# Kernel optimization log

Hardware: AMD Instinct MI355X
Metric: run time of the kernel (lower is better)

Reference implementation:

```python
import jax, jax.numpy as jnp
import numpy as np

D = 64        # GatedGraphConv out_channels
N_LAYERS = 5  # number of stacked convs


def setup_inputs() -> dict:
    key = jax.random.key(0)
    ks = jax.random.split(key, 16)
    N, E, G = 100000, 1600000, 64
    s = 0.1
    inp = {
        'conv_weight': jax.random.normal(ks[0], (N_LAYERS, D, D), jnp.float32) * s,
        'gru_w_ih':    jax.random.normal(ks[1], (N_LAYERS, 3 * D, D), jnp.float32) * s,
        'gru_w_hh':    jax.random.normal(ks[2], (N_LAYERS, 3 * D, D), jnp.float32) * s,
        'gru_b_ih':    jax.random.normal(ks[3], (N_LAYERS, 3 * D), jnp.float32) * s,
        'gru_b_hh':    jax.random.normal(ks[4], (N_LAYERS, 3 * D), jnp.float32) * s,
        'fc1_w': jax.random.normal(ks[5], (32, D), jnp.float32) * s,
        'fc1_b': jax.random.normal(ks[6], (32,), jnp.float32) * s,
        'fc2_w': jax.random.normal(ks[7], (16, 32), jnp.float32) * s,
        'fc2_b': jax.random.normal(ks[8], (16,), jnp.float32) * s,
        'fc3_w': jax.random.normal(ks[9], (1, 16), jnp.float32) * s,
        'fc3_b': jax.random.normal(ks[10], (1,), jnp.float32) * s,
        'edge_index': jax.random.randint(ks[11], (2, E), 0, N, jnp.int64 if jax.config.jax_enable_x64 else jnp.int32),
        'batch': jnp.sort(jax.random.randint(ks[12], (N,), 0, G, jnp.int32)),
        'num_nodes': N,
        'num_graphs': G,
    }
    return inp


def _gru_cell(m, h, w_ih, w_hh, b_ih, b_hh):
    # torch.nn.GRUCell math; m: [N,D] input, h: [N,D] hidden
    gi = m @ w_ih.T + b_ih   # [N, 3D]
    gh = h @ w_hh.T + b_hh   # [N, 3D]
    i_r, i_z, i_n = jnp.split(gi, 3, axis=1)
    h_r, h_z, h_n = jnp.split(gh, 3, axis=1)
    r = jax.nn.sigmoid(i_r + h_r)
    z = jax.nn.sigmoid(i_z + h_z)
    n = jnp.tanh(i_n + r * h_n)
    return (1.0 - z) * n + z * h


def reference(conv_weight, gru_w_ih, gru_w_hh, gru_b_ih, gru_b_hh,
              fc1_w, fc1_b, fc2_w, fc2_b, fc3_w, fc3_b,
              edge_index, batch, num_nodes, num_graphs):
    src, dst = edge_index[0], edge_index[1]  # source_to_target flow
    # initial node features: zeros [N,8] zero-padded to D by GatedGraphConv
    x0 = jnp.zeros((num_nodes, D), jnp.float32)

    def step(x, params):
        w, wih, whh, bih, bhh = params
        m = x @ w                                        # [N, D]
        agg = jax.ops.segment_sum(m[src], dst, num_segments=num_nodes)  # scatter-add
        return _gru_cell(agg, x, wih, whh, bih, bhh), None

    x, _ = jax.lax.scan(step, x0,
                        (conv_weight, gru_w_ih, gru_w_hh, gru_b_ih, gru_b_hh))

    # scatter_add pooling over batch -> [num_graphs, D]
    g = jax.ops.segment_sum(x, batch, num_segments=num_graphs)
    h = jax.nn.elu(g @ fc1_w.T + fc1_b)
    h = jax.nn.elu(h @ fc2_w.T + fc2_b)
    return h @ fc3_w.T + fc3_b  # [num_graphs, 1]
```

## Files before the change

### kernel.cpp

```cpp
#include <hip/hip_runtime.h>
#include <math.h>

typedef _Float16 f16x2 __attribute__((ext_vector_type(2)));
typedef _Float16 f16x4 __attribute__((ext_vector_type(4)));
typedef _Float16 f16x8 __attribute__((ext_vector_type(8)));
typedef float f32x4 __attribute__((ext_vector_type(4)));

#define CBITS 10
#define FCHUNK 4096
#define MATSZ 13056
__device__ __forceinline__ int woff(int row) { return 64 * row + 8 * (row >> 1); }

__device__ __forceinline__ float sigmoidf_(float v) {
  return 1.0f / (1.0f + __expf(-v));
}
__device__ __forceinline__ float tanhf_(float v) {
  v = fminf(fmaxf(v, -15.f), 15.f);
  float e = __expf(2.f * v);
  return (e - 1.f) / (e + 1.f);
}
__device__ __forceinline__ float eluf_(float v) { return v > 0.f ? v : (__expf(v) - 1.f); }

__global__ __launch_bounds__(256) void fuse_w_kernel(const float* __restrict__ conv_w,
                                                     const float* __restrict__ w_ih,
                                                     _Float16* __restrict__ wcS) {
  const int l = blockIdx.x >> 2;
  const int j0 = (blockIdx.x & 3) * 48;
  const float* W = conv_w + (size_t)l * 4096;
  const float* wi = w_ih + (size_t)l * 12288;
  _Float16* out = wcS + (size_t)l * MATSZ;
  __shared__ float sWt[64 * 68];
  __shared__ float sI[48 * 64];
  const int t = threadIdx.x;
  for (int i = t; i < 4096; i += 256) sWt[(i & 63) * 68 + (i >> 6)] = W[i];
  for (int i = t; i < 3072; i += 256) sI[i] = wi[j0 * 64 + i];
  __syncthreads();
#pragma unroll
  for (int r = 0; r < 3; ++r) {
    int u = t + 256 * r;
    int j = u >> 4, cg = (u & 15) * 4;
    float4 a = {0.f, 0.f, 0.f, 0.f};
    for (int k = 0; k < 64; ++k) {
      float4 w = *(const float4*)(sWt + k * 68 + cg);
      float s = sI[j * 64 + k];
      a.x += w.x * s; a.y += w.y * s; a.z += w.z * s; a.w += w.w * s;
    }
    int row = j0 + j;
    f16x4 hv;
    hv[0] = (_Float16)a.x; hv[1] = (_Float16)a.y;
    hv[2] = (_Float16)a.z; hv[3] = (_Float16)a.w;
    *(f16x4*)(out + woff(row) + cg) = hv;
  }
}

__global__ __launch_bounds__(256) void whh_prep_kernel(const float* __restrict__ whh,
                                                       _Float16* __restrict__ whhS) {
  int idx = blockIdx.x * 256 + threadIdx.x;
  if (idx >= 15360) return;
  int l = idx / 3072, rem = idx % 3072;
  int r = rem >> 4, c4 = (rem & 15) * 4;
  float4 v = *(const float4*)(whh + (size_t)l * 12288 + r * 64 + c4);
  f16x4 hv;
  hv[0] = (_Float16)v.x; hv[1] = (_Float16)v.y;
  hv[2] = (_Float16)v.z; hv[3] = (_Float16)v.w;
  *(f16x4*)(whhS + (size_t)l * MATSZ + woff(r) + c4) = hv;
}

__global__ __launch_bounds__(256) void bucket_hist_kernel(const int* __restrict__ dst,
                                                          int* __restrict__ bh, int E) {
  __shared__ int h[128];
  const int t = threadIdx.x;
  if (t < 128) h[t] = 0;
  __syncthreads();
  for (int e = blockIdx.x * 256 + t; e < E; e += gridDim.x * 256)
    atomicAdd(&h[dst[e] >> CBITS], 1);
  __syncthreads();
  if (t < 128 && h[t]) atomicAdd(&bh[t * 16], h[t]);
}

__global__ __launch_bounds__(128) void bucket_scan_kernel(int* __restrict__ bh, int nbk,
                                                          int* __restrict__ boffs, int E) {
  __shared__ int s[128];
  const int t = threadIdx.x;
  int v = (t < nbk) ? bh[t * 16] : 0;
  s[t] = v;
  __syncthreads();
  for (int o = 1; o < 128; o <<= 1) {
    int a = (t >= o) ? s[t - o] : 0;
    __syncthreads();
    s[t] += a;
    __syncthreads();
  }
  if (t < nbk) {
    int ex = s[t] - v;
    boffs[t] = ex;
    bh[t * 16] = ex;
  }
  if (t == 0) boffs[nbk] = E;
}

__global__ __launch_bounds__(256) void bucket_fill_kernel(const int* __restrict__ src,
                                                          const int* __restrict__ dst,
                                                          int* __restrict__ bcur,
                                                          unsigned* __restrict__ pairs, int E) {
  __shared__ uint2 staged[FCHUNK];
  __shared__ int h[128], lbase[128], gbase[128], lcur[128];
  const int t = threadIdx.x;
  const int e0 = blockIdx.x * FCHUNK;
  int cnt = E - e0;
  if (cnt > FCHUNK) cnt = FCHUNK;
  if (t < 128) h[t] = 0;
  __syncthreads();
  for (int i = t; i < cnt; i += 256) atomicAdd(&h[dst[e0 + i] >> CBITS], 1);
  __syncthreads();
  if (t < 128) lcur[t] = h[t];
  __syncthreads();
  for (int o = 1; o < 128; o <<= 1) {
    int a = 0;
    if (t < 128 && t >= o) a = lcur[t - o];
    __syncthreads();
    if (t < 128) lcur[t] += a;
    __syncthreads();
  }
  if (t < 128) {
    int ex = lcur[t] - h[t];
    lbase[t] = ex;
    if (h[t]) gbase[t] = atomicAdd(&bcur[t * 16], h[t]);
    lcur[t] = ex;
  }
  __syncthreads();
  for (int i = t; i < cnt; i += 256) {
    int d = dst[e0 + i];
    int b = d >> CBITS;
    int p = atomicAdd(&lcur[b], 1);
    staged[p] = make_uint2((unsigned)src[e0 + i], (unsigned)d);
  }
  __syncthreads();
  for (int i = t; i < cnt; i += 256) {
    uint2 pr = staged[i];
    int b = (int)(pr.y >> CBITS);
    pairs[gbase[b] + (i - lbase[b])] = (pr.x << CBITS) | (pr.y & ((1u << CBITS) - 1));
  }
}

__global__ __launch_bounds__(256) void csr_build_kernel(const unsigned* __restrict__ pairs,
                                                        const int* __restrict__ boffs,
                                                        int* __restrict__ offs,
                                                        int* __restrict__ srcs, int N, int E) {
  const int b = blockIdx.x, t = threadIdx.x;
  const int nbase = b << CBITS;
  __shared__ int deg[1024];
  __shared__ int ssc[256];
  for (int i = t; i < 1024; i += 256) deg[i] = 0;
  __syncthreads();
  const int beg = boffs[b], end = boffs[b + 1];
  for (int e = beg + t; e < end; e += 256) atomicAdd(&deg[pairs[e] & 1023], 1);
  __syncthreads();
  int d0 = deg[4 * t], d1 = deg[4 * t + 1], d2 = deg[4 * t + 2], d3 = deg[4 * t + 3];
  int s = d0 + d1 + d2 + d3;
  ssc[t] = s;
  __syncthreads();
  for (int o = 1; o < 256; o <<= 1) {
    int a = (t >= o) ? ssc[t - o] : 0;
    __syncthreads();
    ssc[t] += a;
    __syncthreads();
  }
  int base = beg + ssc[t] - s;
  int c0 = base, c1 = c0 + d0, c2 = c1 + d1, c3 = c2 + d2;
  if (nbase + 4 * t + 0 < N) offs[nbase + 4 * t + 0] = c0;
  if (nbase + 4 * t + 1 < N) offs[nbase + 4 * t + 1] = c1;
  if (nbase + 4 * t + 2 < N) offs[nbase + 4 * t + 2] = c2;
  if (nbase + 4 * t + 3 < N) offs[nbase + 4 * t + 3] = c3;
  deg[4 * t] = c0; deg[4 * t + 1] = c1; deg[4 * t + 2] = c2; deg[4 * t + 3] = c3;
  if (b == 0 && t == 0) offs[N] = E;
  if (b == 0 && t < 64) srcs[E + t] = 0;
  __syncthreads();
  for (int e = beg + t; e < end; e += 256) {
    unsigned p = pairs[e];
    int pos = atomicAdd(&deg[p & 1023], 1);
    srcs[pos] = (int)(p >> CBITS);
  }
}

__global__ __launch_bounds__(64) void h1_kernel(const float* __restrict__ b_ih,
                                                const float* __restrict__ b_hh,
                                                float* __restrict__ h1) {
  int d = threadIdx.x;
  float r = sigmoidf_(b_ih[d] + b_hh[d]);
  float z = sigmoidf_(b_ih[64 + d] + b_hh[64 + d]);
  float n = tanhf_(b_ih[128 + d] + r * b_hh[128 + d]);
  h1[d] = (1.f - z) * n;
}

__global__ __launch_bounds__(256) void bcast_kernel(const int* __restrict__ offs,
                                                    const float* __restrict__ h1,
                                                    _Float16* __restrict__ xh,
                                                    _Float16* __restrict__ aggh,
                                                    int N, int units) {
  int idx = blockIdx.x * 256 + threadIdx.x;
  if (idx >= units) return;
  int v = idx >> 5, lp = idx & 31;
  float2 hh = *(const float2*)(h1 + lp * 2);
  f16x2 hv;
  hv[0] = (_Float16)hh.x; hv[1] = (_Float16)hh.y;
  *(f16x2*)(xh + (size_t)idx * 2) = hv;
  float dg = (v < N) ? (float)(offs[v + 1] - offs[v]) : 0.f;
  f16x2 av;
  av[0] = (_Float16)(dg * hh.x); av[1] = (_Float16)(dg * hh.y);
  *(f16x2*)(aggh + (size_t)idx * 2) = av;
}

__global__ __launch_bounds__(256) void agg_kernel(const _Float16* __restrict__ xh,
                                                  const int* __restrict__ offs,
                                                  const int* __restrict__ srcs,
                                                  _Float16* __restrict__ aggh, int N) {
  int wave = threadIdx.x >> 6, lane = threadIdx.x & 63;
  int v = blockIdx.x * 4 + wave;
  if (v >= N) return;
  const int beg = offs[v], end = offs[v + 1];
  const int deg = end - beg;
  const int og = lane >> 3;
  const int lp = lane & 7;
  f16x8 acc = {};
  for (int base = 0; base < deg; base += 64) {
    const int cnt = min(64, deg - base);
    int sidx = srcs[beg + base + lane];
    for (int e = 0; e < cnt; e += 8) {
      int me = e + og;
      int s = __shfl(sidx, me);
      f16x8 vv = *(const f16x8*)(xh + (size_t)s * 64 + lp * 8);
      if (me < cnt) acc += vv;
    }
  }
#pragma unroll
  for (int off = 8; off < 64; off <<= 1) {
    union { f16x8 h; int i[4]; } a, b;
    a.h = acc;
#pragma unroll
    for (int w = 0; w < 4; ++w) b.i[w] = __shfl_xor(a.i[w], off);
    acc += b.h;
  }
  if (og == 0) *(f16x8*)(aggh + (size_t)v * 64 + lp * 8) = acc;
}

__global__ __launch_bounds__(256) void gru_kernel(const _Float16* __restrict__ aggh,
                                                  const _Float16* __restrict__ xh_in,
                                                  _Float16* __restrict__ xh_out,
                                                  const _Float16* __restrict__ wcS,
                                                  const _Float16* __restrict__ whhS,
                                                  const float* __restrict__ b_ih,
                                                  const float* __restrict__ b_hh,
                                                  int N, int numIter) {
  __shared__ _Float16 sW[2 * MATSZ];
  const int t = threadIdx.x;
  for (int i = t; i < 2 * (MATSZ / 8); i += 256) {
    int mat = (i >= MATSZ / 8);
    int idx = i - mat * (MATSZ / 8);
    *(f16x8*)(sW + mat * MATSZ + idx * 8) =
        *(const f16x8*)((mat ? whhS : wcS) + idx * 8);
  }
  __syncthreads();
  const int wave = t >> 6, lane = t & 63;
  const int q = lane >> 4, c = lane & 15;
  float bRZ[4], bZZ[4], bIN[4], bHN[4];
#pragma unroll
  for (int dt = 0; dt < 4; ++dt) {
    int d = dt * 16 + c;
    bRZ[dt] = b_ih[d] + b_hh[d];
    bZZ[dt] = b_ih[64 + d] + b_hh[64 + d];
    bIN[dt] = b_ih[128 + d];
    bHN[dt] = b_hh[128 + d];
  }
  f16x8 idf[2];
#pragma unroll
  for (int p = 0; p < 2; ++p) {
    int tgt = p * 16 + c - q * 8;
#pragma unroll
    for (int j = 0; j < 8; ++j) idf[p][j] = (j == tgt) ? (_Float16)1.0f : (_Float16)0.0f;
  }
#pragma unroll 1
  for (int it = blockIdx.x; it < numIter; it += gridDim.x) {
    const int tile = it >> 1, half = it & 1;
    const int nb0 = tile * 64 + wave * 16;
    const size_t rowbase = (size_t)(nb0 + c) * 64;
    f16x8 aA[2], aH[2];
#pragma unroll
    for (int ks = 0; ks < 2; ++ks) {
      aA[ks] = *(const f16x8*)(aggh + rowbase + ks * 32 + q * 8);
      aH[ks] = *(const f16x8*)(xh_in + rowbase + ks * 32 + q * 8);
    }
    f32x4 aR[2], aZ[2], aN[2], aHNa[2], aHO[2];
#pragma unroll
    for (int p = 0; p < 2; ++p) {
      float brz = half ? bRZ[2 + p] : bRZ[p];
      float bzz = half ? bZZ[2 + p] : bZZ[p];
      float bin = half ? bIN[2 + p] : bIN[p];
      float bhn = half ? bHN[2 + p] : bHN[p];
      aR[p] = (f32x4){brz, brz, brz, brz};
      aZ[p] = (f32x4){bzz, bzz, bzz, bzz};
      aN[p] = (f32x4){bin, bin, bin, bin};
      aHNa[p] = (f32x4){bhn, bhn, bhn, bhn};
      aHO[p] = (f32x4){0.f, 0.f, 0.f, 0.f};
    }
#pragma unroll
    for (int ks = 0; ks < 2; ++ks) {
      const int colo = ks * 32 + q * 8;
#pragma unroll
      for (int p = 0; p < 2; ++p) {
        const int r0 = (half * 2 + p) * 16 + c;
        f16x8 bWr = *(const f16x8*)(sW + woff(r0) + colo);
        f16x8 bHr = *(const f16x8*)(sW + MATSZ + woff(r0) + colo);
        f16x8 bWz = *(const f16x8*)(sW + woff(64 + r0) + colo);
        f16x8 bHz = *(const f16x8*)(sW + MATSZ + woff(64 + r0) + colo);
        f16x8 bWn = *(const f16x8*)(sW + woff(128 + r0) + colo);
        f16x8 bHn = *(const f16x8*)(sW + MATSZ + woff(128 + r0) + colo);
        aR[p] = __builtin_amdgcn_mfma_f32_16x16x32_f16(aA[ks], bWr, aR[p], 0, 0, 0);
        aR[p] = __builtin_amdgcn_mfma_f32_16x16x32_f16(aH[ks], bHr, aR[p], 0, 0, 0);
        aZ[p] = __builtin_amdgcn_mfma_f32_16x16x32_f16(aA[ks], bWz, aZ[p], 0, 0, 0);
        aZ[p] = __builtin_amdgcn_mfma_f32_16x16x32_f16(aH[ks], bHz, aZ[p], 0, 0, 0);
        aN[p] = __builtin_amdgcn_mfma_f32_16x16x32_f16(aA[ks], bWn, aN[p], 0, 0, 0);
        aHNa[p] = __builtin_amdgcn_mfma_f32_16x16x32_f16(aH[ks], bHn, aHNa[p], 0, 0, 0);
      }
    }
#pragma unroll
    for (int p = 0; p < 2; ++p)
      aHO[p] = __builtin_amdgcn_mfma_f32_16x16x32_f16(aH[half], idf[p], aHO[p], 0, 0, 0);
#pragma unroll
    for (int p = 0; p < 2; ++p) {
      int d = (half * 2 + p) * 16 + c;
#pragma unroll
      for (int r = 0; r < 4; ++r) {
        int node = nb0 + q * 4 + r;
        if (node < N) {
          float rr = sigmoidf_(aR[p][r]);
          float zz = sigmoidf_(aZ[p][r]);
          float nn = tanhf_(aN[p][r] + rr * aHNa[p][r]);
          float out = nn + zz * (aHO[p][r] - nn);
          xh_out[(size_t)node * 64 + d] = (_Float16)out;
        }
      }
    }
  }
}

__global__ __launch_bounds__(256) void pool_kernel(const _Float16* __restrict__ xh,
                                                   const int* __restrict__ batch,
                                                   float* __restrict__ g, int N) {
  int wave = threadIdx.x >> 6, lane = threadIdx.x & 63;
  int n0 = blockIdx.x * 64 + wave * 16;
  if (n0 >= N) return;
  int end = n0 + 16;
  if (end > N) end = N;
  int cur = batch[n0];
  float acc = 0.f;
  for (int n = n0; n < end; ++n) {
    int b = batch[n];
    if (b != cur) {
      atomicAdd(&g[(size_t)cur * 64 + lane], acc);
      acc = 0.f;
      cur = b;
    }
    acc += (float)xh[(size_t)n * 64 + lane];
  }
  atomicAdd(&g[(size_t)cur * 64 + lane], acc);
}

__global__ __launch_bounds__(256) void mlp_kernel(const float* __restrict__ g,
                                                  const float* __restrict__ w1,
                                                  const float* __restrict__ b1,
                                                  const float* __restrict__ w2,
                                                  const float* __restrict__ b2,
                                                  const float* __restrict__ w3,
                                                  const float* __restrict__ b3,
                                                  float* __restrict__ out, int G) {
  __shared__ float sG[64 * 64];
  __shared__ float sH1[64 * 32];
  __shared__ float sH2[64 * 16];
  int t = threadIdx.x;
  for (int i = t; i < G * 64; i += 256) sG[i] = g[i];
  __syncthreads();
  for (int o = t; o < G * 32; o += 256) {
    int gi = o >> 5, i = o & 31;
    float a = b1[i];
    for (int k = 0; k < 64; ++k) a += sG[gi * 64 + k] * w1[i * 64 + k];
    sH1[gi * 32 + i] = eluf_(a);
  }
  __syncthreads();
  for (int o = t; o < G * 16; o += 256) {
    int gi = o >> 4, i = o & 15;
    float a = b2[i];
    for (int k = 0; k < 32; ++k) a += sH1[gi * 32 + k] * w2[i * 32 + k];
    sH2[gi * 16 + i] = eluf_(a);
  }
  __syncthreads();
  for (int o = t; o < G; o += 256) {
    float a = b3[0];
    for (int k = 0; k < 16; ++k) a += sH2[o * 16 + k] * w3[k];
    out[o] = a;
  }
}

extern "C" void kernel_launch(void* const* d_in, const int* in_sizes, int n_in,
                              void* d_out, int out_size, void* d_ws, size_t ws_size,
                              hipStream_t stream) {
  const float* conv_w = (const float*)d_in[0];
  const float* w_ih = (const float*)d_in[1];
  const float* w_hh = (const float*)d_in[2];
  const float* b_ih = (const float*)d_in[3];
  const float* b_hh = (const float*)d_in[4];
  const float* fc1_w = (const float*)d_in[5];
  const float* fc1_b = (const float*)d_in[6];
  const float* fc2_w = (const float*)d_in[7];
  const float* fc2_b = (const float*)d_in[8];
  const float* fc3_w = (const float*)d_in[9];
  const float* fc3_b = (const float*)d_in[10];
  const int* ei = (const int*)d_in[11];
  const int* batch = (const int*)d_in[12];
  const int N = in_sizes[12];
  const int E = in_sizes[11] / 2;
  const int G = out_size;
  const int* src = ei;
  const int* dst = ei + E;
  const int nbk = (N + 1023) >> CBITS;
  const int tiles = (N + 63) / 64;
  const int Npad = tiles * 64;
  const int gruIter = tiles * 2;

  char* ws = (char*)d_ws;
  size_t off = 0;
  auto alloc = [&](size_t bytes) -> void* {
    void* p = ws + off;
    off += (bytes + 255) & ~(size_t)255;
    return p;
  };
  _Float16* xhA = (_Float16*)alloc((size_t)Npad * 64 * 2);
  _Float16* xhB = (_Float16*)alloc((size_t)Npad * 64 * 2);
  _Float16* aggh = (_Float16*)alloc((size_t)Npad * 64 * 2);
  _Float16* wcS = (_Float16*)alloc((size_t)5 * MATSZ * 2);
  _Float16* whhS = (_Float16*)alloc((size_t)5 * MATSZ * 2);
  float* h1 = (float*)alloc(64 * 4);
  float* gbuf = (float*)alloc((size_t)G * 64 * 4);
  int* offs = (int*)alloc((size_t)(N + 1) * 4);
  int* srcs = (int*)alloc((size_t)(E + 64) * 4);
  unsigned* pairs = (unsigned*)alloc((size_t)E * 4);
  int* bh = (int*)alloc(128 * 16 * 4);
  int* boffs = (int*)alloc(129 * 4);

  hipMemsetAsync(bh, 0, 128 * 16 * 4, stream);
  bucket_hist_kernel<<<256, 256, 0, stream>>>(dst, bh, E);
  bucket_scan_kernel<<<1, 128, 0, stream>>>(bh, nbk, boffs, E);
  bucket_fill_kernel<<<(E + FCHUNK - 1) / FCHUNK, 256, 0, stream>>>(src, dst, bh, pairs, E);
  csr_build_kernel<<<nbk, 256, 0, stream>>>(pairs, boffs, offs, srcs, N, E);

  fuse_w_kernel<<<20, 256, 0, stream>>>(conv_w, w_ih, wcS);
  whh_prep_kernel<<<60, 256, 0, stream>>>(w_hh, whhS);

  h1_kernel<<<1, 64, 0, stream>>>(b_ih, b_hh, h1);
  bcast_kernel<<<(Npad * 32 + 255) / 256, 256, 0, stream>>>(offs, h1, xhA, aggh, N, Npad * 32);

  _Float16* cur = xhA;
  _Float16* nxt = xhB;
  gru_kernel<<<768, 256, 0, stream>>>(aggh, cur, nxt, wcS + MATSZ, whhS + MATSZ,
                                      b_ih + 192, b_hh + 192, N, gruIter);
  { _Float16* tmp = cur; cur = nxt; nxt = tmp; }
  for (int l = 2; l < 5; ++l) {
    agg_kernel<<<(N + 3) / 4, 256, 0, stream>>>(cur, offs, srcs, aggh, N);
    gru_kernel<<<768, 256, 0, stream>>>(aggh, cur, nxt, wcS + (size_t)l * MATSZ,
                                        whhS + (size_t)l * MATSZ, b_ih + (size_t)l * 192,
                                        b_hh + (size_t)l * 192, N, gruIter);
    _Float16* tmp = cur; cur = nxt; nxt = tmp;
  }

  hipMemsetAsync(gbuf, 0, (size_t)G * 64 * 4, stream);
  pool_kernel<<<(N + 63) / 64, 256, 0, stream>>>(cur, batch, gbuf, N);
  mlp_kernel<<<1, 256, 0, stream>>>(gbuf, fc1_w, fc1_b, fc2_w, fc2_b, fc3_w, fc3_b,
                                    (float*)d_out, G);
}
```

Measured before the change: 423.4 us.

## Compute second GRU layer in closed form from node degree, skipping its GEMM

Every node enters layer 1 with the same hidden state h1, so each node's aggregate is just its degree times h1. Layer 1's GRU pre-activations are therefore affine in degree. A tiny kernel precomputes the per-gate vectors u and constants. An elementwise kernel then evaluates the GRU output per node from its degree alone. This replaces the broadcast write of agg plus a full GRU GEMM launch, at the cost of sigmoid and tanh work per element and slightly different fp16 rounding.

```diff
diff --git a/kernel.cpp b/kernel.cpp
--- a/kernel.cpp
+++ b/kernel.cpp
@@ -193,22 +193,51 @@
   h1[d] = (1.f - z) * n;
 }
 
-__global__ __launch_bounds__(256) void bcast_kernel(const int* __restrict__ offs,
-                                                    const float* __restrict__ h1,
-                                                    _Float16* __restrict__ xh,
-                                                    _Float16* __restrict__ aggh,
-                                                    int N, int units) {
+__global__ __launch_bounds__(256) void l1u_kernel(const _Float16* __restrict__ wcS1,
+                                                  const _Float16* __restrict__ whhS1,
+                                                  const float* __restrict__ h1,
+                                                  const float* __restrict__ b_ih1,
+                                                  const float* __restrict__ b_hh1,
+                                                  float* __restrict__ u,
+                                                  float* __restrict__ cons) {
+  int j = threadIdx.x;
+  if (j >= 192) return;
+  float su = 0.f, sg = 0.f;
+  const int base = woff(j);
+  for (int c = 0; c < 64; ++c) {
+    float hc = h1[c];
+    su += hc * (float)wcS1[base + c];
+    sg += hc * (float)whhS1[base + c];
+  }
+  u[j] = su;
+  if (j < 128) {
+    cons[j] = sg + b_ih1[j] + b_hh1[j];
+  } else {
+    cons[j] = b_ih1[j];
+    cons[j + 64] = sg + b_hh1[j];
+  }
+}
+
+__global__ __launch_bounds__(256) void l1_elem_kernel(const int* __restrict__ offs,
+                                                      const float* __restrict__ h1,
+                                                      const float* __restrict__ u,
+                                                      const float* __restrict__ cons,
+                                                      _Float16* __restrict__ xh,
+                                                      int N, int units) {
   int idx = blockIdx.x * 256 + threadIdx.x;
   if (idx >= units) return;
   int v = idx >> 5, lp = idx & 31;
-  float2 hh = *(const float2*)(h1 + lp * 2);
-  f16x2 hv;
-  hv[0] = (_Float16)hh.x; hv[1] = (_Float16)hh.y;
-  *(f16x2*)(xh + (size_t)idx * 2) = hv;
   float dg = (v < N) ? (float)(offs[v + 1] - offs[v]) : 0.f;
-  f16x2 av;
-  av[0] = (_Float16)(dg * hh.x); av[1] = (_Float16)(dg * hh.y);
-  *(f16x2*)(aggh + (size_t)idx * 2) = av;
+  f16x2 o;
+#pragma unroll
+  for (int k = 0; k < 2; ++k) {
+    int d = 2 * lp + k;
+    float r = sigmoidf_(dg * u[d] + cons[d]);
+    float z = sigmoidf_(dg * u[64 + d] + cons[64 + d]);
+    float n = tanhf_(dg * u[128 + d] + cons[128 + d] + r * cons[192 + d]);
+    o[k] = (_Float16)(n + z * (h1[d] - n));
+  }
+  *(f16x2*)(xh + (size_t)idx * 2) = o;
 }
 
 __global__ __launch_bounds__(256) void agg_kernel(const _Float16* __restrict__ xh,
@@ -440,6 +469,8 @@
   _Float16* wcS = (_Float16*)alloc((size_t)5 * MATSZ * 2);
   _Float16* whhS = (_Float16*)alloc((size_t)5 * MATSZ * 2);
   float* h1 = (float*)alloc(64 * 4);
+  float* l1u = (float*)alloc(192 * 4);
+  float* l1c = (float*)alloc(256 * 4);
   float* gbuf = (float*)alloc((size_t)G * 64 * 4);
   int* offs = (int*)alloc((size_t)(N + 1) * 4);
   int* srcs = (int*)alloc((size_t)(E + 64) * 4);
@@ -457,13 +488,13 @@
   whh_prep_kernel<<<60, 256, 0, stream>>>(w_hh, whhS);
 
   h1_kernel<<<1, 64, 0, stream>>>(b_ih, b_hh, h1);
-  bcast_kernel<<<(Npad * 32 + 255) / 256, 256, 0, stream>>>(offs, h1, xhA, aggh, N, Npad * 32);
+  l1u_kernel<<<1, 256, 0, stream>>>(wcS + MATSZ, whhS + MATSZ, h1,
+                                    b_ih + 192, b_hh + 192, l1u, l1c);
+  l1_elem_kernel<<<(Npad * 32 + 255) / 256, 256, 0, stream>>>(offs, h1, l1u, l1c, xhA,
+                                                              N, Npad * 32);
 
   _Float16* cur = xhA;
   _Float16* nxt = xhB;
-  gru_kernel<<<768, 256, 0, stream>>>(aggh, cur, nxt, wcS + MATSZ, whhS + MATSZ,
-                                      b_ih + 192, b_hh + 192, N, gruIter);
-  { _Float16* tmp = cur; cur = nxt; nxt = tmp; }
   for (int l = 2; l < 5; ++l) {
     agg_kernel<<<(N + 3) / 4, 256, 0, stream>>>(cur, offs, srcs, aggh, N);
     gru_kernel<<<768, 256, 0, stream>>>(aggh, cur, nxt, wcS + (size_t)l * MATSZ,
```

Result: faster. 409.5 us (-3.3%).
